# Kernel optimization log

Hardware: AMD Instinct MI355X
Metric: run time of the kernel (lower is better)

## Reference

```python
import jax, jax.numpy as jnp
import numpy as np

NUM_NODES = 50000
NUM_EDGES = 800000
NUM_FEATURES = 128
HIDDEN = 256
NUM_CLASSES = 10
NUM_GRAPHS = 64


def setup_inputs() -> dict:
    key = jax.random.key(0)
    ks = jax.random.split(key, 16)
    x = jax.random.normal(ks[0], (NUM_NODES, NUM_FEATURES), dtype=jnp.float32)
    edge_index = jax.random.randint(ks[1], (2, NUM_EDGES), 0, NUM_NODES, dtype=jnp.int64)
    batch = jnp.sort(jax.random.randint(ks[2], (NUM_NODES,), 0, NUM_GRAPHS, dtype=jnp.int64))

    def glorot(k, shape):
        fan_in, fan_out = shape[-2], shape[-1]
        s = jnp.sqrt(6.0 / (fan_in + fan_out)).astype(jnp.float32)
        return jax.random.uniform(k, shape, jnp.float32, -s, s)

    inp = {
        "x": x, "edge_index": edge_index, "batch": batch,
        # Chebyshev weights: one [in, out] matrix per hop order k
        "W1": glorot(ks[3], (3, NUM_FEATURES, HIDDEN)), "b1": jnp.zeros((HIDDEN,), jnp.float32),
        "W2": glorot(ks[4], (4, HIDDEN, HIDDEN)),       "b2": jnp.zeros((HIDDEN,), jnp.float32),
        "W3": glorot(ks[5], (5, HIDDEN, HIDDEN)),       "b3": jnp.zeros((HIDDEN,), jnp.float32),
        "fc1_w": glorot(ks[6], (HIDDEN, 512)),  "fc1_b": jnp.zeros((512,), jnp.float32),
        "fc2_w": glorot(ks[7], (512, HIDDEN)),  "fc2_b": jnp.zeros((HIDDEN,), jnp.float32),
        "fc3_w": glorot(ks[8], (HIDDEN, NUM_CLASSES)), "fc3_b": jnp.zeros((NUM_CLASSES,), jnp.float32),
    }
    return inp


def reference(x, edge_index, batch, W1, b1, W2, b2, W3, b3,
              fc1_w, fc1_b, fc2_w, fc2_b, fc3_w, fc3_b):
    N = x.shape[0]
    src, dst = edge_index[0], edge_index[1]

    # Scaled Laplacian L_hat = -D^{-1/2} A D^{-1/2} (lambda_max = 2, sym norm)
    deg = jax.ops.segment_sum(jnp.ones_like(src, dtype=x.dtype), src, num_segments=N)
    dis = jnp.where(deg > 0, jax.lax.rsqrt(jnp.maximum(deg, 1.0)), 0.0)
    w = -dis[src] * dis[dst]  # [E]

    def prop(h):  # L_hat @ h via gather-scale-scatter
        return jax.ops.segment_sum(h[src] * w[:, None], dst, num_segments=N)

    def cheb(h, Wk, b):
        K = Wk.shape[0]
        Tx0 = h
        out = Tx0 @ Wk[0]
        Tx1 = prop(h)
        out = out + Tx1 @ Wk[1]
        for k in range(2, K):
            Tx2 = 2.0 * prop(Tx1) - Tx0
            out = out + Tx2 @ Wk[k]
            Tx0, Tx1 = Tx1, Tx2
        return out + b

    h = jax.nn.relu(cheb(x, W1, b1))
    h = jax.nn.relu(cheb(h, W2, b2))
    h = jax.nn.relu(cheb(h, W3, b3))

    # global mean pool over graphs in the batch
    sums = jax.ops.segment_sum(h, batch, num_segments=NUM_GRAPHS)
    cnts = jax.ops.segment_sum(jnp.ones((N,), h.dtype), batch, num_segments=NUM_GRAPHS)
    g = sums / jnp.maximum(cnts, 1.0)[:, None]  # [G, 256]

    g = jax.nn.relu(g @ fc1_w + fc1_b)  # dropout is identity at inference
    g = jax.nn.relu(g @ fc2_w + fc2_b)
    g = g @ fc3_w + fc3_b
    return jax.nn.log_softmax(g, axis=1)
```

## Files before the change

### kernel.cpp

```cpp
#include <hip/hip_runtime.h>
#include <cstdint>
#include <cstddef>

#define NN 50000
#define NE 800000
#define FIN 128
#define HID 256
#define NCLS 10
#define NG 64
#define LDT 1280

#define NCH 13
#define NCELL (NN * NCH)
#define NSCB ((NCELL + 255) / 256)
#define NDISB ((NN + 255) / 256)

#define FB 3125
#define WTB 2688
#define SXB 12500

typedef unsigned int uint;
typedef unsigned short ushort;
typedef __attribute__((ext_vector_type(8))) short short8;
typedef __attribute__((ext_vector_type(4))) float f32x4;

static inline size_t align_up(size_t v, size_t a) { return (v + a - 1) / a * a; }

__device__ __forceinline__ float bf2f(ushort u) {
    union { uint i; float f; } v; v.i = (uint)u << 16; return v.f;
}
__device__ __forceinline__ ushort f2bf(float f) {
    union { uint i; float f; } v; v.f = f;
    uint i = v.i;
    uint r = (i + 0x7fffu + ((i >> 16) & 1u)) >> 16;
    return (ushort)r;
}
__device__ __forceinline__ uint pack2(float a, float b) {
    return (uint)f2bf(a) | ((uint)f2bf(b) << 16);
}


__global__ void k_degcnt(const int* __restrict__ src, const int* __restrict__ dst,
                         int* __restrict__ ideg, uint* __restrict__ cellcnt32,
                         ushort* __restrict__ rank16) {
    int e = blockIdx.x * 256 + threadIdx.x;
    if (e < NE) {
        int s = src[e], d = dst[e];
        atomicAdd(&ideg[s], 1);
        int cell = d * NCH + (s >> 12);
        uint old = atomicAdd(&cellcnt32[cell >> 1], 1u << ((cell & 1) * 16));
        rank16[e] = (ushort)((old >> ((cell & 1) * 16)) & 0xffffu);
    }
}

__global__ void k_scanA_dis(const uint* __restrict__ cnt32, int* __restrict__ rp,
                            int* __restrict__ bsum, const int* __restrict__ ideg,
                            float* __restrict__ dis) {
    if (blockIdx.x >= NSCB) {
        int n = (blockIdx.x - NSCB) * 256 + threadIdx.x;
        if (n < NN) {
            int d = ideg[n];
            dis[n] = (d > 0) ? rsqrtf((float)d) : 0.0f;
        }
        return;
    }
    __shared__ int s[256];
    int i = blockIdx.x * 256 + threadIdx.x;
    int v = 0;
    if (i < NCELL) v = (int)((cnt32[i >> 1] >> ((i & 1) * 16)) & 0xffffu);
    s[threadIdx.x] = v;
    __syncthreads();
    for (int off = 1; off < 256; off <<= 1) {
        int t = (threadIdx.x >= (unsigned)off) ? s[threadIdx.x - off] : 0;
        __syncthreads();
        s[threadIdx.x] += t;
        __syncthreads();
    }
    if (i < NCELL) rp[i] = s[threadIdx.x] - v;
    if (threadIdx.x == 255) bsum[blockIdx.x] = s[255];
}

__global__ void k_scanB(int* __restrict__ b, int n) {
    __shared__ int s[1024];
    __shared__ int carry;
    if (threadIdx.x == 0) carry = 0;
    __syncthreads();
    for (int base = 0; base < n; base += 1024) {
        int i = base + threadIdx.x;
        int v = (i < n) ? b[i] : 0;
        s[threadIdx.x] = v;
        __syncthreads();
        for (int off = 1; off < 1024; off <<= 1) {
            int t = (threadIdx.x >= (unsigned)off) ? s[threadIdx.x - off] : 0;
            __syncthreads();
            s[threadIdx.x] += t;
            __syncthreads();
        }
        int c = carry;
        if (i < n) b[i] = c + s[threadIdx.x] - v;
        __syncthreads();
        if (threadIdx.x == 0) carry = c + s[1023];
        __syncthreads();
    }
}

__global__ void k_scanC(const int* __restrict__ bsum, int* __restrict__ rp,
                        int* __restrict__ rpn) {
    int i = blockIdx.x * 256 + threadIdx.x;
    if (i < NCELL) {
        int v = rp[i] + bsum[blockIdx.x];
        rp[i] = v;
        if (i % NCH == 0) rpn[i / NCH] = v;
    }
    if (i == 0) rpn[NN] = NE;
}

__global__ void k_fused_prep(
    const int* __restrict__ src, const int* __restrict__ dst,
    const float* __restrict__ dis, const int* __restrict__ cellptr,
    const ushort* __restrict__ rank16, uint2* __restrict__ em,
    const float* __restrict__ W1, const float* __restrict__ W2,
    const float* __restrict__ W3, ushort* __restrict__ Wt1,
    ushort* __restrict__ Wt2, ushort* __restrict__ Wt3,
    const float* __restrict__ x, ushort* __restrict__ T) {
    int b = blockIdx.x;
    if (b < FB) {
        int e = b * 256 + threadIdx.x;
        if (e < NE) {
            int s = src[e], d = dst[e];
            int cell = d * NCH + (s >> 12);
            int pos = cellptr[cell] + (int)rank16[e];
            uint2 m;
            m.x = (uint)s;
            m.y = __float_as_uint(-dis[s] * dis[d]);
            em[pos] = m;
        }
        return;
    }
    if (b < FB + WTB) {
        int i = (b - FB) * 256 + threadIdx.x;
        if (i < 384 * 256) {
            int k = i >> 8, n = i & 255;
            Wt1[(size_t)n * 384 + k] = f2bf(W1[i]);
            return;
        }
        i -= 384 * 256;
        if (i < 1024 * 256) {
            int k = i >> 8, n = i & 255;
            Wt2[(size_t)n * 1024 + k] = f2bf(W2[i]);
            return;
        }
        i -= 1024 * 256;
        if (i < 1280 * 256) {
            int k = i >> 8, n = i & 255;
            Wt3[(size_t)n * 1280 + k] = f2bf(W3[i]);
        }
        return;
    }
    int i = (b - FB - WTB) * 256 + threadIdx.x;
    if (i < NN * 64) {
        int m = i >> 6, p = i & 63;
        const float* xp = x + (size_t)m * FIN + p * 2;
        uint* tp = (uint*)(T + (size_t)m * LDT) + p;
        *tp = pack2(xp[0], xp[1]);
    }
}

template <int FUSE, int F>
__global__ __launch_bounds__(512) void k_prop3(
    const int* __restrict__ rpn, const uint2* __restrict__ em,
    const ushort* __restrict__ h, const ushort* __restrict__ sub,
    ushort* __restrict__ out) {
    constexpr int NV = (F == 256) ? 4 : 2;
    int wv = __builtin_amdgcn_readfirstlane(threadIdx.x >> 6);
    int d = blockIdx.x * 8 + wv;
    int lane = threadIdx.x & 63;
    int beg = rpn[d], end = rpn[d + 1];
    float a[NV];
#pragma unroll
    for (int j = 0; j < NV; ++j) a[j] = 0.0f;

    int e = beg;
    int nfull = (end - beg) >> 3;
    if (nfull > 0) {
        uint2 mt[8];
#pragma unroll
        for (int u = 0; u < 8; ++u) mt[u] = em[e + u];
        for (int g = 0; g < nfull; ++g) {
            uint2 mtn[8];
            if (F == 256) {
                uint2 gg[8];
#pragma unroll
                for (int u = 0; u < 8; ++u)
                    gg[u] = *((const uint2*)(h + (size_t)mt[u].x * LDT) + lane);
#pragma unroll
                for (int u = 0; u < 8; ++u) {
                    int pe = e + 8 + u; if (pe > end - 1) pe = end - 1;
                    mtn[u] = em[pe];
                }
#pragma unroll
                for (int u = 0; u < 8; ++u) {
                    float wvv = __uint_as_float(mt[u].y);
                    a[0] += wvv * bf2f((ushort)gg[u].x);
                    a[1] += wvv * bf2f((ushort)(gg[u].x >> 16));
                    a[2] += wvv * bf2f((ushort)gg[u].y);
                    a[3] += wvv * bf2f((ushort)(gg[u].y >> 16));
                }
            } else {
                uint gg[8];
#pragma unroll
                for (int u = 0; u < 8; ++u)
                    gg[u] = *((const uint*)(h + (size_t)mt[u].x * LDT) + lane);
#pragma unroll
                for (int u = 0; u < 8; ++u) {
                    int pe = e + 8 + u; if (pe > end - 1) pe = end - 1;
                    mtn[u] = em[pe];
                }
#pragma unroll
                for (int u = 0; u < 8; ++u) {
                    float wvv = __uint_as_float(mt[u].y);
                    a[0] += wvv * bf2f((ushort)gg[u]);
                    a[1] += wvv * bf2f((ushort)(gg[u] >> 16));
                }
            }
#pragma unroll
            for (int u = 0; u < 8; ++u) mt[u] = mtn[u];
            e += 8;
        }
    }
    for (; e + 4 <= end; e += 4) {
        uint2 mt[4];
#pragma unroll
        for (int u = 0; u < 4; ++u) mt[u] = em[e + u];
        if (F == 256) {
            uint2 gg[4];
#pragma unroll
            for (int u = 0; u < 4; ++u)
                gg[u] = *((const uint2*)(h + (size_t)mt[u].x * LDT) + lane);
#pragma unroll
            for (int u = 0; u < 4; ++u) {
                float wvv = __uint_as_float(mt[u].y);
                a[0] += wvv * bf2f((ushort)gg[u].x);
                a[1] += wvv * bf2f((ushort)(gg[u].x >> 16));
                a[2] += wvv * bf2f((ushort)gg[u].y);
                a[3] += wvv * bf2f((ushort)(gg[u].y >> 16));
            }
        } else {
            uint gg[4];
#pragma unroll
            for (int u = 0; u < 4; ++u)
                gg[u] = *((const uint*)(h + (size_t)mt[u].x * LDT) + lane);
#pragma unroll
            for (int u = 0; u < 4; ++u) {
                float wvv = __uint_as_float(mt[u].y);
                a[0] += wvv * bf2f((ushort)gg[u]);
                a[1] += wvv * bf2f((ushort)(gg[u] >> 16));
            }
        }
    }
    for (; e < end; ++e) {
        uint2 m0 = em[e];
        float w0 = __uint_as_float(m0.y);
        if (F == 256) {
            uint2 g0 = *((const uint2*)(h + (size_t)m0.x * LDT) + lane);
            a[0] += w0 * bf2f((ushort)g0.x); a[1] += w0 * bf2f((ushort)(g0.x >> 16));
            a[2] += w0 * bf2f((ushort)g0.y); a[3] += w0 * bf2f((ushort)(g0.y >> 16));
        } else {
            uint g0 = *((const uint*)(h + (size_t)m0.x * LDT) + lane);
            a[0] += w0 * bf2f((ushort)g0); a[1] += w0 * bf2f((ushort)(g0 >> 16));
        }
    }

    if (F == 256) {
        uint2* op = (uint2*)(out + (size_t)d * LDT) + lane;
        if (FUSE) {
            uint2 sv = *((const uint2*)(sub + (size_t)d * LDT) + lane);
            uint2 r;
            r.x = pack2(2.0f * a[0] - bf2f((ushort)sv.x),
                        2.0f * a[1] - bf2f((ushort)(sv.x >> 16)));
            r.y = pack2(2.0f * a[2] - bf2f((ushort)sv.y),
                        2.0f * a[3] - bf2f((ushort)(sv.y >> 16)));
            *op = r;
        } else {
            uint2 r;
            r.x = pack2(a[0], a[1]);
            r.y = pack2(a[2], a[3]);
            *op = r;
        }
    } else {
        uint* op = (uint*)(out + (size_t)d * LDT) + lane;
        if (FUSE) {
            uint sv = *((const uint*)(sub + (size_t)d * LDT) + lane);
            *op = pack2(2.0f * a[0] - bf2f((ushort)sv),
                        2.0f * a[1] - bf2f((ushort)(sv >> 16)));
        } else {
            *op = pack2(a[0], a[1]);
        }
    }
}

template <int K>
__global__ __launch_bounds__(512, 4) void k_mm7(
    const ushort* __restrict__ A, int lda,
    int m0, int m1, int m2, int m3, int m4,
    const ushort* __restrict__ Wt, const float* __restrict__ bias,
    ushort* __restrict__ H, int ldh, int M) {
    constexpr int NT = K / 32;
    __shared__ ushort As[3][128 * 32];
    __shared__ ushort Bs[3][256 * 32];
    int tid = threadIdx.x;
    int lane = tid & 63, w = tid >> 6;
    int wm = w >> 2, wn = w & 3;
    int rowBase = blockIdx.x * 128;
    int srow = lane >> 2;
    int c16 = lane & 3;

    f32x4 acc[4][4];
#pragma unroll
    for (int i = 0; i < 4; ++i)
#pragma unroll
        for (int j = 0; j < 4; ++j) acc[i][j] = (f32x4){0.f, 0.f, 0.f, 0.f};

    auto stage = [&](int t) {
        int kk = t * 32;
        int slot = kk >> 8;
        int coff = (slot == 0 ? m0 : slot == 1 ? m1 : slot == 2 ? m2
                    : slot == 3 ? m3 : m4) + (kk & 255);
        int b = t % 3;
        {
            int r = w * 16 + srow;
            int cs = c16 ^ ((r >> 1) & 3);
            int grow = rowBase + r;
            if (grow > M - 1) grow = M - 1;
            const ushort* gp = A + (size_t)grow * lda + coff + cs * 8;
            __builtin_amdgcn_global_load_lds(
                (const __attribute__((address_space(1))) void*)gp,
                (__attribute__((address_space(3))) void*)((char*)&As[b][0] + w * 1024),
                16, 0, 0);
        }
#pragma unroll
        for (int q = 0; q < 2; ++q) {
            int seg = w * 2 + q;
            int r = seg * 16 + srow;
            int cs = c16 ^ ((r >> 1) & 3);
            const ushort* gp = Wt + (size_t)r * K + kk + cs * 8;
            __builtin_amdgcn_global_load_lds(
                (const __attribute__((address_space(1))) void*)gp,
                (__attribute__((address_space(3))) void*)((char*)&Bs[b][0] + seg * 1024),
                16, 0, 0);
        }
    };

    stage(0);
    stage(1);

    for (int t = 0; t < NT; ++t) {
        if (t + 1 < NT) {
            asm volatile("s_waitcnt vmcnt(3)" ::: "memory");
        } else {
            asm volatile("s_waitcnt vmcnt(0)" ::: "memory");
        }
        __builtin_amdgcn_s_barrier();
        if (t + 2 < NT) stage(t + 2);

        int b = t % 3;
        short8 af[4], bf[4];
#pragma unroll
        for (int mi = 0; mi < 4; ++mi) {
            int r = wm * 64 + mi * 16 + (lane & 15);
            int j = (lane >> 4) ^ ((r >> 1) & 3);
            af[mi] = *(const short8*)((const char*)&As[b][0] + r * 64 + j * 16);
        }
#pragma unroll
        for (int ni = 0; ni < 4; ++ni) {
            int r = wn * 64 + ni * 16 + (lane & 15);
            int j = (lane >> 4) ^ ((r >> 1) & 3);
            bf[ni] = *(const short8*)((const char*)&Bs[b][0] + r * 64 + j * 16);
        }
#pragma unroll
        for (int mi = 0; mi < 4; ++mi)
#pragma unroll
            for (int ni = 0; ni < 4; ++ni)
                acc[mi][ni] = __builtin_amdgcn_mfma_f32_16x16x32_bf16(
                    af[mi], bf[ni], acc[mi][ni], 0, 0, 0);
    }

    int lg = lane >> 4;
    float bv[4];
#pragma unroll
    for (int ni = 0; ni < 4; ++ni)
        bv[ni] = bias[wn * 64 + ni * 16 + (lane & 15)];
#pragma unroll
    for (int mi = 0; mi < 4; ++mi) {
#pragma unroll
        for (int r = 0; r < 4; ++r) {
            int row = rowBase + wm * 64 + mi * 16 + lg * 4 + r;
            if (row >= M) continue;
#pragma unroll
            for (int ni = 0; ni < 4; ++ni) {
                int colL = wn * 64 + ni * 16 + (lane & 15);
                float v = acc[mi][ni][r] + bv[ni];
                v = fmaxf(v, 0.0f);
                H[(size_t)row * ldh + colL] = f2bf(v);
            }
        }
    }
}


__global__ void k_pool(const ushort* __restrict__ h, const int* __restrict__ batch,
                       float* __restrict__ sums, float* __restrict__ cnts) {
    int f = threadIdx.x;
    int n0 = blockIdx.x * 128;
    if (n0 >= NN) return;
    int nEnd = n0 + 128 < NN ? n0 + 128 : NN;
    int cur = batch[n0];
    float acc = 0.0f, c = 0.0f;
    for (int n = n0; n < nEnd; ++n) {
        int b = batch[n];
        if (b != cur) {
            atomicAdd(&sums[cur * HID + f], acc);
            if (f == 0) atomicAdd(&cnts[cur], c);
            acc = 0.0f; c = 0.0f; cur = b;
        }
        acc += bf2f(h[(size_t)n * HID + f]);
        c += 1.0f;
    }
    atomicAdd(&sums[cur * HID + f], acc);
    if (f == 0) atomicAdd(&cnts[cur], c);
}

__global__ void k_gdiv(const float* __restrict__ sums, const float* __restrict__ cnts,
                       float* __restrict__ g) {
    int i = blockIdx.x * 256 + threadIdx.x;
    int b = i >> 8;
    g[i] = sums[i] / fmaxf(cnts[b], 1.0f);
}


template <int RELU>
__global__ void k_fc(const float* __restrict__ in, const float* __restrict__ W,
                     const float* __restrict__ bias, float* __restrict__ out,
                     int K, int Nc) {
    __shared__ float s[512];
    int gi = blockIdx.x;
    for (int i = threadIdx.x; i < K; i += blockDim.x) s[i] = in[gi * K + i];
    __syncthreads();
    int c = blockIdx.y * blockDim.x + threadIdx.x;
    if (c < Nc) {
        float acc = bias[c];
        for (int k = 0; k < K; ++k) acc += s[k] * W[k * Nc + c];
        out[gi * Nc + c] = RELU ? fmaxf(acc, 0.0f) : acc;
    }
}

__global__ void k_fc3_lsm(const float* __restrict__ in, const float* __restrict__ W,
                          const float* __restrict__ b, float* __restrict__ out) {
    __shared__ float s[HID];
    __shared__ float lg[NCLS];
    int gi = blockIdx.x;
    s[threadIdx.x] = in[gi * HID + threadIdx.x];
    __syncthreads();
    if (threadIdx.x < NCLS) {
        float acc = b[threadIdx.x];
        for (int k = 0; k < HID; ++k) acc += s[k] * W[k * NCLS + threadIdx.x];
        lg[threadIdx.x] = acc;
    }
    __syncthreads();
    if (threadIdx.x < NCLS) {
        float m = -1e30f;
        for (int c = 0; c < NCLS; ++c) m = fmaxf(m, lg[c]);
        float sum = 0.0f;
        for (int c = 0; c < NCLS; ++c) sum += expf(lg[c] - m);
        out[gi * NCLS + threadIdx.x] = lg[threadIdx.x] - m - logf(sum);
    }
}


extern "C" void kernel_launch(void* const* d_in, const int* in_sizes, int n_in,
                              void* d_out, int out_size, void* d_ws, size_t ws_size,
                              hipStream_t stream) {
    const float* x = (const float*)d_in[0];
    const int* ei = (const int*)d_in[1];
    const int* src = ei;
    const int* dst = ei + NE;
    const int* batch = (const int*)d_in[2];
    const float* W1 = (const float*)d_in[3];
    const float* b1 = (const float*)d_in[4];
    const float* W2 = (const float*)d_in[5];
    const float* b2 = (const float*)d_in[6];
    const float* W3 = (const float*)d_in[7];
    const float* b3 = (const float*)d_in[8];
    const float* fc1w = (const float*)d_in[9];
    const float* fc1b = (const float*)d_in[10];
    const float* fc2w = (const float*)d_in[11];
    const float* fc2b = (const float*)d_in[12];
    const float* fc3w = (const float*)d_in[13];
    const float* fc3b = (const float*)d_in[14];
    float* out = (float*)d_out;

    char* p = (char*)d_ws;
    auto carve = [&](size_t bytes) {
        char* r = p;
        p += align_up(bytes, 256);
        return (void*)r;
    };
    ushort* Tbig = (ushort*)carve((size_t)NN * LDT * 2);
    ushort* hA = (ushort*)carve((size_t)NN * HID * 2);
    ushort* Wt1 = (ushort*)carve((size_t)HID * 384 * 2);
    ushort* Wt2 = (ushort*)carve((size_t)HID * 1024 * 2);
    ushort* Wt3 = (ushort*)carve((size_t)HID * 1280 * 2);
    int* ideg = (int*)carve((size_t)NN * 4);
    float* dis = (float*)carve((size_t)NN * 4);
    uint2* em = (uint2*)carve((size_t)NE * 8);
    uint* cellcnt32 = (uint*)carve((size_t)NCELL * 2);
    int* cellptr = (int*)carve((size_t)(NCELL + 1) * 4);
    ushort* rank16 = (ushort*)carve((size_t)NE * 2);
    int* rpn = (int*)carve((size_t)(NN + 1) * 4);
    int* bsum = (int*)carve((size_t)NSCB * 4);
    float* psum = (float*)carve((size_t)NG * HID * 4);
    float* pcnt = (float*)carve((size_t)NG * 4);
    float* g = (float*)carve((size_t)NG * HID * 4);
    float* f1 = (float*)carve((size_t)NG * 512 * 4);
    float* f2 = (float*)carve((size_t)NG * HID * 4);

    hipMemsetAsync(ideg, 0, (size_t)NN * 4, stream);
    hipMemsetAsync(cellcnt32, 0, (size_t)NCELL * 2, stream);
    hipMemsetAsync(psum, 0, (size_t)NG * HID * 4, stream);
    hipMemsetAsync(pcnt, 0, (size_t)NG * 4, stream);

    k_degcnt<<<(NE + 255) / 256, 256, 0, stream>>>(src, dst, ideg, cellcnt32, rank16);
    k_scanA_dis<<<NSCB + NDISB, 256, 0, stream>>>(cellcnt32, cellptr, bsum, ideg, dis);
    k_scanB<<<1, 1024, 0, stream>>>(bsum, NSCB);
    k_scanC<<<NSCB, 256, 0, stream>>>(bsum, cellptr, rpn);
    k_fused_prep<<<FB + WTB + SXB, 256, 0, stream>>>(
        src, dst, dis, cellptr, rank16, em,
        W1, W2, W3, Wt1, Wt2, Wt3, x, Tbig);

    int mmg = (NN + 127) / 128;

    k_prop3<0, 128><<<NN / 8, 512, 0, stream>>>(rpn, em, Tbig + 0, nullptr, Tbig + 128);
    k_prop3<1, 128><<<NN / 8, 512, 0, stream>>>(rpn, em, Tbig + 128, Tbig + 0, Tbig + 256);
    k_mm7<384><<<mmg, 512, 0, stream>>>(Tbig, LDT, 0, 256, 0, 0, 0,
                                        Wt1, b1, Tbig + 1024, LDT, NN);

    k_prop3<0, 256><<<NN / 8, 512, 0, stream>>>(rpn, em, Tbig + 1024, nullptr, Tbig + 0);
    k_prop3<1, 256><<<NN / 8, 512, 0, stream>>>(rpn, em, Tbig + 0, Tbig + 1024, Tbig + 256);
    k_prop3<1, 256><<<NN / 8, 512, 0, stream>>>(rpn, em, Tbig + 256, Tbig + 0, Tbig + 512);
    k_mm7<1024><<<mmg, 512, 0, stream>>>(Tbig, LDT, 1024, 0, 256, 512, 0,
                                         Wt2, b2, Tbig + 768, LDT, NN);

    k_prop3<0, 256><<<NN / 8, 512, 0, stream>>>(rpn, em, Tbig + 768, nullptr, Tbig + 1024);
    k_prop3<1, 256><<<NN / 8, 512, 0, stream>>>(rpn, em, Tbig + 1024, Tbig + 768, Tbig + 0);
    k_prop3<1, 256><<<NN / 8, 512, 0, stream>>>(rpn, em, Tbig + 0, Tbig + 1024, Tbig + 256);
    k_prop3<1, 256><<<NN / 8, 512, 0, stream>>>(rpn, em, Tbig + 256, Tbig + 0, Tbig + 512);
    k_mm7<1280><<<mmg, 512, 0, stream>>>(Tbig, LDT, 768, 1024, 0, 256, 512,
                                         Wt3, b3, hA, HID, NN);

    k_pool<<<(NN + 127) / 128, 256, 0, stream>>>(hA, batch, psum, pcnt);
    k_gdiv<<<(NG * HID) / 256, 256, 0, stream>>>(psum, pcnt, g);
    k_fc<1><<<dim3(NG, 2), 256, 0, stream>>>(g, fc1w, fc1b, f1, HID, 512);
    k_fc<1><<<dim3(NG, 1), 256, 0, stream>>>(f1, fc2w, fc2b, f2, 512, HID);
    k_fc3_lsm<<<NG, 256, 0, stream>>>(f2, fc3w, fc3b, out);
}
```

Before: 781.7 us.

## Reorder destination nodes by degree bins for propagation load balance

Adds a degree histogram, a prefix scan and a permutation so the propagation kernels process destination nodes grouped by degree. The goal is to reduce wave imbalance inside blocks. The prep kernels are also regrouped: the counting step is merged with the weight and x conversion, and edge filling becomes a separate kernel. The binning uses source out-degree rather than destination in-degree. It also adds indirection and breaks sequential destination order, which hurts output and edge-array locality.

```diff
diff --git a/kernel.cpp b/kernel.cpp
--- a/kernel.cpp
+++ b/kernel.cpp
@@ -15,7 +15,7 @@
 #define NSCB ((NCELL + 255) / 256)
 #define NDISB ((NN + 255) / 256)
 
-#define FB 3125
+#define DB 3125
 #define WTB 2688
 #define SXB 12500
 
@@ -39,28 +39,65 @@
     return (uint)f2bf(a) | ((uint)f2bf(b) << 16);
 }
 
-
-__global__ void k_degcnt(const int* __restrict__ src, const int* __restrict__ dst,
-                         int* __restrict__ ideg, uint* __restrict__ cellcnt32,
-                         ushort* __restrict__ rank16) {
-    int e = blockIdx.x * 256 + threadIdx.x;
-    if (e < NE) {
-        int s = src[e], d = dst[e];
-        atomicAdd(&ideg[s], 1);
-        int cell = d * NCH + (s >> 12);
-        uint old = atomicAdd(&cellcnt32[cell >> 1], 1u << ((cell & 1) * 16));
-        rank16[e] = (ushort)((old >> ((cell & 1) * 16)) & 0xffffu);
+__global__ void k_prep1(
+    const int* __restrict__ src, const int* __restrict__ dst,
+    int* __restrict__ ideg, uint* __restrict__ cellcnt32,
+    ushort* __restrict__ rank16,
+    const float* __restrict__ W1, const float* __restrict__ W2,
+    const float* __restrict__ W3, ushort* __restrict__ Wt1,
+    ushort* __restrict__ Wt2, ushort* __restrict__ Wt3,
+    const float* __restrict__ x, ushort* __restrict__ T) {
+    int b = blockIdx.x;
+    if (b < DB) {
+        int e = b * 256 + threadIdx.x;
+        if (e < NE) {
+            int s = src[e], d = dst[e];
+            atomicAdd(&ideg[s], 1);
+            int cell = d * NCH + (s >> 12);
+            uint old = atomicAdd(&cellcnt32[cell >> 1], 1u << ((cell & 1) * 16));
+            rank16[e] = (ushort)((old >> ((cell & 1) * 16)) & 0xffffu);
+        }
+        return;
+    }
+    if (b < DB + WTB) {
+        int i = (b - DB) * 256 + threadIdx.x;
+        if (i < 384 * 256) {
+            int k = i >> 8, n = i & 255;
+            Wt1[(size_t)n * 384 + k] = f2bf(W1[i]);
+            return;
+        }
+        i -= 384 * 256;
+        if (i < 1024 * 256) {
+            int k = i >> 8, n = i & 255;
+            Wt2[(size_t)n * 1024 + k] = f2bf(W2[i]);
+            return;
+        }
+        i -= 1024 * 256;
+        if (i < 1280 * 256) {
+            int k = i >> 8, n = i & 255;
+            Wt3[(size_t)n * 1280 + k] = f2bf(W3[i]);
+        }
+        return;
+    }
+    int i = (b - DB - WTB) * 256 + threadIdx.x;
+    if (i < NN * 64) {
+        int m = i >> 6, p = i & 63;
+        const float* xp = x + (size_t)m * FIN + p * 2;
+        uint* tp = (uint*)(T + (size_t)m * LDT) + p;
+        *tp = pack2(xp[0], xp[1]);
     }
 }
 
 __global__ void k_scanA_dis(const uint* __restrict__ cnt32, int* __restrict__ rp,
                             int* __restrict__ bsum, const int* __restrict__ ideg,
-                            float* __restrict__ dis) {
+                            float* __restrict__ dis, int* __restrict__ dbin) {
     if (blockIdx.x >= NSCB) {
         int n = (blockIdx.x - NSCB) * 256 + threadIdx.x;
         if (n < NN) {
             int d = ideg[n];
             dis[n] = (d > 0) ? rsqrtf((float)d) : 0.0f;
+            int bin = d < 63 ? d : 63;
+            atomicAdd(&dbin[bin], 1);
         }
         return;
     }
@@ -80,7 +117,7 @@
     if (threadIdx.x == 255) bsum[blockIdx.x] = s[255];
 }
 
-__global__ void k_scanB(int* __restrict__ b, int n) {
+__global__ void k_scanB(int* __restrict__ b, int n, int* __restrict__ dbin) {
     __shared__ int s[1024];
     __shared__ int carry;
     if (threadIdx.x == 0) carry = 0;
@@ -102,10 +139,25 @@
         if (threadIdx.x == 0) carry = c + s[1023];
         __syncthreads();
     }
+    if (threadIdx.x == 0) {
+        int acc = 0;
+        for (int i = 0; i < 64; ++i) { int t = dbin[i]; dbin[i] = acc; acc += t; }
+    }
 }
 
 __global__ void k_scanC(const int* __restrict__ bsum, int* __restrict__ rp,
-                        int* __restrict__ rpn) {
+                        int* __restrict__ rpn, const int* __restrict__ ideg,
+                        int* __restrict__ dbin, int* __restrict__ perm) {
+    if (blockIdx.x >= NSCB) {
+        int n = (blockIdx.x - NSCB) * 256 + threadIdx.x;
+        if (n < NN) {
+            int d = ideg[n];
+            int bin = d < 63 ? d : 63;
+            int pos = atomicAdd(&dbin[bin], 1);
+            perm[pos] = n;
+        }
+        return;
+    }
     int i = blockIdx.x * 256 + threadIdx.x;
     if (i < NCELL) {
         int v = rp[i] + bsum[blockIdx.x];
@@ -115,65 +167,30 @@
     if (i == 0) rpn[NN] = NE;
 }
 
-__global__ void k_fused_prep(
-    const int* __restrict__ src, const int* __restrict__ dst,
-    const float* __restrict__ dis, const int* __restrict__ cellptr,
-    const ushort* __restrict__ rank16, uint2* __restrict__ em,
-    const float* __restrict__ W1, const float* __restrict__ W2,
-    const float* __restrict__ W3, ushort* __restrict__ Wt1,
-    ushort* __restrict__ Wt2, ushort* __restrict__ Wt3,
-    const float* __restrict__ x, ushort* __restrict__ T) {
-    int b = blockIdx.x;
-    if (b < FB) {
-        int e = b * 256 + threadIdx.x;
-        if (e < NE) {
-            int s = src[e], d = dst[e];
-            int cell = d * NCH + (s >> 12);
-            int pos = cellptr[cell] + (int)rank16[e];
-            uint2 m;
-            m.x = (uint)s;
-            m.y = __float_as_uint(-dis[s] * dis[d]);
-            em[pos] = m;
-        }
-        return;
-    }
-    if (b < FB + WTB) {
-        int i = (b - FB) * 256 + threadIdx.x;
-        if (i < 384 * 256) {
-            int k = i >> 8, n = i & 255;
-            Wt1[(size_t)n * 384 + k] = f2bf(W1[i]);
-            return;
-        }
-        i -= 384 * 256;
-        if (i < 1024 * 256) {
-            int k = i >> 8, n = i & 255;
-            Wt2[(size_t)n * 1024 + k] = f2bf(W2[i]);
-            return;
-        }
-        i -= 1024 * 256;
-        if (i < 1280 * 256) {
-            int k = i >> 8, n = i & 255;
-            Wt3[(size_t)n * 1280 + k] = f2bf(W3[i]);
-        }
-        return;
-    }
-    int i = (b - FB - WTB) * 256 + threadIdx.x;
-    if (i < NN * 64) {
-        int m = i >> 6, p = i & 63;
-        const float* xp = x + (size_t)m * FIN + p * 2;
-        uint* tp = (uint*)(T + (size_t)m * LDT) + p;
-        *tp = pack2(xp[0], xp[1]);
+__global__ void k_fill(const int* __restrict__ src, const int* __restrict__ dst,
+                       const float* __restrict__ dis,
+                       const int* __restrict__ cellptr,
+                       const ushort* __restrict__ rank16, uint2* __restrict__ em) {
+    int e = blockIdx.x * 256 + threadIdx.x;
+    if (e < NE) {
+        int s = src[e], d = dst[e];
+        int cell = d * NCH + (s >> 12);
+        int pos = cellptr[cell] + (int)rank16[e];
+        uint2 m;
+        m.x = (uint)s;
+        m.y = __float_as_uint(-dis[s] * dis[d]);
+        em[pos] = m;
     }
 }
 
 template <int FUSE, int F>
 __global__ __launch_bounds__(512) void k_prop3(
-    const int* __restrict__ rpn, const uint2* __restrict__ em,
-    const ushort* __restrict__ h, const ushort* __restrict__ sub,
-    ushort* __restrict__ out) {
+    const int* __restrict__ perm, const int* __restrict__ rpn,
+    const uint2* __restrict__ em, const ushort* __restrict__ h,
+    const ushort* __restrict__ sub, ushort* __restrict__ out) {
     constexpr int NV = (F == 256) ? 4 : 2;
     int wv = __builtin_amdgcn_readfirstlane(threadIdx.x >> 6);
-    int d = blockIdx.x * 8 + wv;
+    int d = perm[blockIdx.x * 8 + wv];
     int lane = threadIdx.x & 63;
     int beg = rpn[d], end = rpn[d + 1];
     float a[NV];
@@ -518,6 +535,8 @@
     ushort* rank16 = (ushort*)carve((size_t)NE * 2);
     int* rpn = (int*)carve((size_t)(NN + 1) * 4);
     int* bsum = (int*)carve((size_t)NSCB * 4);
+    int* dbin = (int*)carve((size_t)64 * 4);
+    int* perm = (int*)carve((size_t)NN * 4);
     float* psum = (float*)carve((size_t)NG * HID * 4);
     float* pcnt = (float*)carve((size_t)NG * 4);
     float* g = (float*)carve((size_t)NG * HID * 4);
@@ -526,34 +545,36 @@
 
     hipMemsetAsync(ideg, 0, (size_t)NN * 4, stream);
     hipMemsetAsync(cellcnt32, 0, (size_t)NCELL * 2, stream);
+    hipMemsetAsync(dbin, 0, 64 * 4, stream);
     hipMemsetAsync(psum, 0, (size_t)NG * HID * 4, stream);
     hipMemsetAsync(pcnt, 0, (size_t)NG * 4, stream);
 
-    k_degcnt<<<(NE + 255) / 256, 256, 0, stream>>>(src, dst, ideg, cellcnt32, rank16);
-    k_scanA_dis<<<NSCB + NDISB, 256, 0, stream>>>(cellcnt32, cellptr, bsum, ideg, dis);
-    k_scanB<<<1, 1024, 0, stream>>>(bsum, NSCB);
-    k_scanC<<<NSCB, 256, 0, stream>>>(bsum, cellptr, rpn);
-    k_fused_prep<<<FB + WTB + SXB, 256, 0, stream>>>(
-        src, dst, dis, cellptr, rank16, em,
+    k_prep1<<<DB + WTB + SXB, 256, 0, stream>>>(
+        src, dst, ideg, cellcnt32, rank16,
         W1, W2, W3, Wt1, Wt2, Wt3, x, Tbig);
+    k_scanA_dis<<<NSCB + NDISB, 256, 0, stream>>>(cellcnt32, cellptr, bsum,
+                                                  ideg, dis, dbin);
+    k_scanB<<<1, 1024, 0, stream>>>(bsum, NSCB, dbin);
+    k_scanC<<<NSCB + NDISB, 256, 0, stream>>>(bsum, cellptr, rpn, ideg, dbin, perm);
+    k_fill<<<DB, 256, 0, stream>>>(src, dst, dis, cellptr, rank16, em);
 
     int mmg = (NN + 127) / 128;
 
-    k_prop3<0, 128><<<NN / 8, 512, 0, stream>>>(rpn, em, Tbig + 0, nullptr, Tbig + 128);
-    k_prop3<1, 128><<<NN / 8, 512, 0, stream>>>(rpn, em, Tbig + 128, Tbig + 0, Tbig + 256);
+    k_prop3<0, 128><<<NN / 8, 512, 0, stream>>>(perm, rpn, em, Tbig + 0, nullptr, Tbig + 128);
+    k_prop3<1, 128><<<NN / 8, 512, 0, stream>>>(perm, rpn, em, Tbig + 128, Tbig + 0, Tbig + 256);
     k_mm7<384><<<mmg, 512, 0, stream>>>(Tbig, LDT, 0, 256, 0, 0, 0,
                                         Wt1, b1, Tbig + 1024, LDT, NN);
 
-    k_prop3<0, 256><<<NN / 8, 512, 0, stream>>>(rpn, em, Tbig + 1024, nullptr, Tbig + 0);
-    k_prop3<1, 256><<<NN / 8, 512, 0, stream>>>(rpn, em, Tbig + 0, Tbig + 1024, Tbig + 256);
-    k_prop3<1, 256><<<NN / 8, 512, 0, stream>>>(rpn, em, Tbig + 256, Tbig + 0, Tbig + 512);
+    k_prop3<0, 256><<<NN / 8, 512, 0, stream>>>(perm, rpn, em, Tbig + 1024, nullptr, Tbig + 0);
+    k_prop3<1, 256><<<NN / 8, 512, 0, stream>>>(perm, rpn, em, Tbig + 0, Tbig + 1024, Tbig + 256);
+    k_prop3<1, 256><<<NN / 8, 512, 0, stream>>>(perm, rpn, em, Tbig + 256, Tbig + 0, Tbig + 512);
     k_mm7<1024><<<mmg, 512, 0, stream>>>(Tbig, LDT, 1024, 0, 256, 512, 0,
                                          Wt2, b2, Tbig + 768, LDT, NN);
 
-    k_prop3<0, 256><<<NN / 8, 512, 0, stream>>>(rpn, em, Tbig + 768, nullptr, Tbig + 1024);
-    k_prop3<1, 256><<<NN / 8, 512, 0, stream>>>(rpn, em, Tbig + 1024, Tbig + 768, Tbig + 0);
-    k_prop3<1, 256><<<NN / 8, 512, 0, stream>>>(rpn, em, Tbig + 0, Tbig + 1024, Tbig + 256);
-    k_prop3<1, 256><<<NN / 8, 512, 0, stream>>>(rpn, em, Tbig + 256, Tbig + 0, Tbig + 512);
+    k_prop3<0, 256><<<NN / 8, 512, 0, stream>>>(perm, rpn, em, Tbig + 768, nullptr, Tbig + 1024);
+    k_prop3<1, 256><<<NN / 8, 512, 0, stream>>>(perm, rpn, em, Tbig + 1024, Tbig + 768, Tbig + 0);
+    k_prop3<1, 256><<<NN / 8, 512, 0, stream>>>(perm, rpn, em, Tbig + 0, Tbig + 1024, Tbig + 256);
+    k_prop3<1, 256><<<NN / 8, 512, 0, stream>>>(perm, rpn, em, Tbig + 256, Tbig + 0, Tbig + 512);
     k_mm7<1280><<<mmg, 512, 0, stream>>>(Tbig, LDT, 768, 1024, 0, 256, 512,
                                          Wt3, b3, hA, HID, NN);
 
```

Measured after the change: 1.052 ms. 34.6% more time.
